# Kernel tuning notes

Measured on AMD Instinct MI355X. Metric: run time of the kernel, lower is better.

The kernel has to match this reference:

```python
import jax, jax.numpy as jnp
import numpy as np

NUM_HEADS = 8

def setup_inputs() -> dict:
    key = jax.random.key(0)
    ks = jax.random.split(key, 16)
    B, N, M, C = 4, 2048, 2048, 256
    Hd = 4 * C  # mlp hidden = dim * mlp_ratio
    std = 0.02
    x = jax.random.normal(ks[0], (B, N, C), dtype=jnp.float32)
    y = jax.random.normal(ks[1], (B, M, C), dtype=jnp.float32)
    token_types = jax.random.randint(ks[2], (B, N), 0, 2).astype(jnp.int64)
    token_types = token_types.at[0, 0].set(0)  # take the fresh-kv branch
    inp = {
        'x': x, 'y': y, 'token_types': token_types,
        'Wq': jax.random.normal(ks[3], (C, C)) * std,
        'Wkv': jax.random.normal(ks[4], (C, 2 * C)) * std,
        'Ws1': jax.random.normal(ks[5], (C, Hd)) * std,
        'bs1': jnp.zeros((Hd,)),
        'Ws2': jax.random.normal(ks[6], (Hd, C)) * std,
        'bs2': jnp.zeros((C,)),
        'Wl1': jax.random.normal(ks[7], (C, Hd)) * std,
        'bl1': jnp.zeros((Hd,)),
        'Wl2': jax.random.normal(ks[8], (Hd, C)) * std,
        'bl2': jnp.zeros((C,)),
    }
    return inp


def reference(x, y, token_types, Wq, Wkv, Ws1, bs1, Ws2, bs2, Wl1, bl1, Wl2, bl2):
    B, N, C = x.shape
    H = NUM_HEADS
    d = C // H
    scale = d ** -0.5
    # q: [B,H,N,d]
    q = (x @ Wq).reshape(B, N, H, d).transpose(0, 2, 1, 3)
    # kv: [B,M,2,H,d] -> k,v: [B,H,M,d]
    M = y.shape[1]
    kv = (y @ Wkv).reshape(B, M, 2, H, d)
    k = kv[:, :, 0].transpose(0, 2, 1, 3)
    v = kv[:, :, 1].transpose(0, 2, 1, 3)
    attn = jax.nn.softmax(jnp.einsum('bhnd,bhmd->bhnm', q, k) * scale, axis=-1)
    ctx = jnp.einsum('bhnm,bhmd->bhnd', attn, v)  # [B,H,N,d]
    ctx = ctx.transpose(0, 2, 1, 3).reshape(B, N, C)
    # MoE MLP: expert_s for token_type==0, expert_l for token_type==1
    out_s = jax.nn.gelu(ctx @ Ws1 + bs1, approximate=False) @ Ws2 + bs2
    out_l = jax.nn.gelu(ctx @ Wl1 + bl1, approximate=False) @ Wl2 + bl2
    is_l = (token_types == 1)[..., None]
    out = jnp.where(is_l, out_l, out_s)
    return out
```

## Files before the change

kernel.cpp:

```cpp
#include <hip/hip_runtime.h>

typedef unsigned short ushort_t;
typedef __attribute__((ext_vector_type(8))) short bf16x8;
typedef __attribute__((ext_vector_type(4))) short bf16x4;
typedef __attribute__((ext_vector_type(4))) float f32x4;

#define MFMA16(a, b, c) __builtin_amdgcn_mfma_f32_16x16x32_bf16(a, b, c, 0, 0, 0)

typedef const __attribute__((address_space(1))) void gvoid_t;
typedef __attribute__((address_space(3))) void lvoid_t;

__device__ __forceinline__ void glds16(const ushort_t* g, ushort_t* l) {
    __builtin_amdgcn_global_load_lds((gvoid_t*)(const void*)g, (lvoid_t*)(void*)l, 16, 0, 0);
}

__device__ inline ushort_t f2bf(float f) {
    union { float f; unsigned int i; } v;
    v.f = f;
    unsigned int r = v.i + 0x7FFFu + ((v.i >> 16) & 1u);
    return (ushort_t)(r >> 16);
}

__device__ __forceinline__ unsigned int cvtpk_bf16(float lo, float hi) {
    unsigned int r;
    asm("v_cvt_pk_bf16_f32 %0, %1, %2" : "=v"(r) : "v"(lo), "v"(hi));
    return r;
}

__device__ __forceinline__ float fexp2(float x) {
    float r;
    asm("v_exp_f32 %0, %1" : "=v"(r) : "v"(x));
    return r;
}

__device__ __forceinline__ float gelu_fast(float x) {
    float z = x * 0.70710678118654752f;
    float a = fabsf(z);
    float den = 1.0f + 0.3275911f * a;
    float tr;
    asm("v_rcp_f32 %0, %1" : "=v"(tr) : "v"(den));
    float poly = ((((1.061405429f * tr - 1.453152027f) * tr + 1.421413741f) * tr
                   - 0.284496736f) * tr + 0.254829592f) * tr;
    float e = fexp2(-z * z * 1.4426950408889634f);
    float erfa = 1.0f - poly * e;
    float erfv = copysignf(erfa, z);
    return 0.5f * x * (1.0f + erfv);
}

__global__ __launch_bounds__(256) void prep_k(
    const float* Wq, const float* Wkv, const float* Ws1,
    const float* Ws2, const float* Wl1, const float* Wl2,
    const float* x, const float* y, const int* tt,
    ushort_t* WqT, ushort_t* WkvT, ushort_t* Ws1T,
    ushort_t* Ws2T, ushort_t* Wl1T, ushort_t* Wl2T,
    ushort_t* xb, ushort_t* yb,
    int* perm0, int* perm1, int* cnt)
{
    const int job = blockIdx.y;
    const int t = threadIdx.x;
    if (job < 6) {
        __shared__ ushort_t lds[64][65];
        const float* src; ushort_t* dst; int R, Cc;
        switch (job) {
            case 0:  src = Wq;  dst = WqT;  R = 256;  Cc = 256;  break;
            case 1:  src = Wkv; dst = WkvT; R = 256;  Cc = 512;  break;
            case 2:  src = Ws1; dst = Ws1T; R = 256;  Cc = 1024; break;
            case 3:  src = Ws2; dst = Ws2T; R = 1024; Cc = 256;  break;
            case 4:  src = Wl1; dst = Wl1T; R = 256;  Cc = 1024; break;
            default: src = Wl2; dst = Wl2T; R = 1024; Cc = 256;  break;
        }
        const int ctiles = Cc >> 6;
        const int ntiles = (R >> 6) * ctiles;
        for (int tile = blockIdx.x; tile < ntiles; tile += gridDim.x) {
            const int r0 = (tile / ctiles) << 6, c0 = (tile - (tile / ctiles) * ctiles) << 6;
            #pragma unroll
            for (int it = 0; it < 16; ++it) {
                int idx = it * 256 + t;
                int rr = idx >> 6, cc = idx & 63;
                lds[rr][cc] = f2bf(src[(size_t)(r0 + rr) * Cc + c0 + cc]);
            }
            __syncthreads();
            #pragma unroll
            for (int it = 0; it < 16; ++it) {
                int idx = it * 256 + t;
                int rr = idx >> 6, cc = idx & 63;
                dst[(size_t)(c0 + rr) * R + r0 + cc] = lds[cc][rr];
            }
            __syncthreads();
        }
    } else if (job < 8) {
        const float* src = (job == 6) ? x : y;
        ushort_t* dst = (job == 6) ? xb : yb;
        const int tid = blockIdx.x * 256 + t;
        const int nth = gridDim.x * 256;
        for (int i = tid; i < (1 << 18); i += nth) {
            f32x4 a0 = *(const f32x4*)(src + (size_t)i * 8);
            f32x4 a1 = *(const f32x4*)(src + (size_t)i * 8 + 4);
            union { unsigned int u[4]; bf16x8 v; } o;
            o.u[0] = cvtpk_bf16(a0[0], a0[1]);
            o.u[1] = cvtpk_bf16(a0[2], a0[3]);
            o.u[2] = cvtpk_bf16(a1[0], a1[1]);
            o.u[3] = cvtpk_bf16(a1[2], a1[3]);
            *(bf16x8*)(dst + (size_t)i * 8) = o.v;
        }
    } else {
        if (blockIdx.x != 0) return;
        __shared__ int s0[256], s1[256];
        unsigned int mask = 0;
        #pragma unroll
        for (int j = 0; j < 8; ++j) {
            int4 v = *(const int4*)(tt + t * 32 + j * 4);
            mask |= (unsigned int)(v.x & 1) << (j * 4)
                  | (unsigned int)(v.y & 1) << (j * 4 + 1)
                  | (unsigned int)(v.z & 1) << (j * 4 + 2)
                  | (unsigned int)(v.w & 1) << (j * 4 + 3);
        }
        const int c1 = __popc(mask), c0 = 32 - c1;
        s0[t] = c0; s1[t] = c1;
        __syncthreads();
        for (int d = 1; d < 256; d <<= 1) {
            int a0 = 0, a1 = 0;
            if (t >= d) { a0 = s0[t - d]; a1 = s1[t - d]; }
            __syncthreads();
            s0[t] += a0; s1[t] += a1;
            __syncthreads();
        }
        const int tot0 = s0[255], tot1 = s1[255];
        int off0 = s0[t] - c0, off1 = s1[t] - c1;
        #pragma unroll
        for (int j = 0; j < 32; ++j) {
            int row = t * 32 + j;
            if ((mask >> j) & 1) perm1[off1++] = row;
            else                 perm0[off0++] = row;
        }
        for (int i = tot0 + t; i < 8320; i += 256) perm0[i] = 0;
        for (int i = tot1 + t; i < 8320; i += 256) perm1[i] = 0;
        if (t == 0) { cnt[0] = tot0; cnt[1] = tot1; }
    }
}

template<int ACT, int GATHER, int SCATTER, int OUTF32, int VSCATTER>
__device__ __forceinline__ void gemm_body(
    ushort_t* Als, ushort_t* Bls, int vbid,
    const ushort_t* __restrict__ A, const ushort_t* __restrict__ Bt,
    const float* __restrict__ bias, void* __restrict__ Cv,
    const int* __restrict__ perm, const int* __restrict__ ncnt,
    ushort_t* __restrict__ kpk, ushort_t* __restrict__ vpk,
    float oscale, int M, int N, int K, int aRowOff, int outRowOff)
{
    const int t = threadIdx.x;
    const int lane = t & 63, w = t >> 6;
    const int wr = w >> 1, wc = w & 1;
    const int ntn = N >> 7;
    const int mt = vbid / ntn, nt = vbid - mt * ntn;
    const int mbase = mt << 7, nbase = nt << 7;
    const int n16 = lane & 15, g = lane >> 4;

    int ne = M;
    if (GATHER || SCATTER) {
        ne = *ncnt;
        if (mbase >= ne) return;
    }

    int arow[4], skb[4], brow[4];
    #pragma unroll
    for (int j = 0; j < 4; ++j) {
        int p = j * 256 + t;
        int sr = p >> 3;
        skb[j] = (p & 7) ^ (sr & 7);
        brow[j] = sr;
        arow[j] = GATHER ? perm[mbase + sr] : (mbase + sr + aRowOff);
    }

    f32x4 acc[4][4];
    #pragma unroll
    for (int mi = 0; mi < 4; ++mi)
        #pragma unroll
        for (int ni = 0; ni < 4; ++ni) acc[mi][ni] = (f32x4){0.f, 0.f, 0.f, 0.f};

    for (int k0 = 0; k0 < K; k0 += 64) {
        #pragma unroll
        for (int j = 0; j < 4; ++j) {
            glds16(A + (size_t)arow[j] * K + k0 + skb[j] * 8, &Als[(j * 256 + t) * 8]);
            glds16(Bt + (size_t)(nbase + brow[j]) * K + k0 + skb[j] * 8, &Bls[(j * 256 + t) * 8]);
        }
        __syncthreads();
        #pragma unroll
        for (int ks = 0; ks < 2; ++ks) {
            bf16x8 af[4], bfr[4];
            #pragma unroll
            for (int i = 0; i < 4; ++i) {
                const int ar = wr * 64 + i * 16 + n16;
                af[i]  = *(const bf16x8*)&Als[ar * 64 + (((ks << 2) + g) ^ (ar & 7)) * 8];
                const int br = wc * 64 + i * 16 + n16;
                bfr[i] = *(const bf16x8*)&Bls[br * 64 + (((ks << 2) + g) ^ (br & 7)) * 8];
            }
            #pragma unroll
            for (int mi = 0; mi < 4; ++mi)
                #pragma unroll
                for (int ni = 0; ni < 4; ++ni)
                    acc[mi][ni] = MFMA16(af[mi], bfr[ni], acc[mi][ni]);
        }
        __syncthreads();
    }

    float bv[4];
    #pragma unroll
    for (int ni = 0; ni < 4; ++ni)
        bv[ni] = (bias != nullptr) ? bias[nbase + wc * 64 + ni * 16 + n16] : 0.f;

    #pragma unroll
    for (int mi = 0; mi < 4; ++mi) {
        #pragma unroll
        for (int r = 0; r < 4; ++r) {
            const int pos = mbase + wr * 64 + mi * 16 + (g << 2) + r;
            int orow = pos + outRowOff;
            if (GATHER || SCATTER) {
                if (pos >= ne) continue;
                if (SCATTER) orow = perm[pos];
            }
            #pragma unroll
            for (int ni = 0; ni < 4; ++ni) {
                const int col = nbase + wc * 64 + ni * 16 + n16;
                float v = (acc[mi][ni][r] + bv[ni]) * oscale;
                if (ACT) v = gelu_fast(v);
                if (VSCATTER) {
                    const int bb = pos >> 11, mm = pos & 2047;
                    if (col < 256) {
                        const int hh = col >> 5, dd = col & 31;
                        kpk[((size_t)(bb * 8 + hh) * 2048 + mm) * 32 + dd] = f2bf(v);
                    } else {
                        const int hh = (col - 256) >> 5, dd = (col - 256) & 31;
                        const int m31 = mm & 31;
                        const int kap = ((m31 >> 2) & 3) * 8 + ((m31 >> 4) & 1) * 4 + (m31 & 3);
                        vpk[(((size_t)(bb * 8 + hh) * 64 + (mm >> 5)) * 32 + dd) * 32 + kap] = f2bf(v);
                    }
                } else {
                    if (OUTF32) ((float*)Cv)[(size_t)orow * N + col] = v;
                    else ((ushort_t*)Cv)[(size_t)orow * N + col] = f2bf(v);
                }
            }
        }
    }
}

__global__ __launch_bounds__(256, 2) void qkv_k(
    const ushort_t* xb, const ushort_t* yb,
    const ushort_t* WqT, const ushort_t* WkvT,
    ushort_t* qws, ushort_t* kpk, ushort_t* vpk, float qscale)
{
    __shared__ ushort_t Als[128 * 64];
    __shared__ ushort_t Bls[128 * 64];
    if (blockIdx.x < 128) {
        gemm_body<0, 0, 0, 0, 0>(Als, Bls, blockIdx.x, xb, WqT, nullptr, qws,
                                 nullptr, nullptr, nullptr, nullptr,
                                 qscale, 8192, 256, 256, 0, 0);
    } else {
        gemm_body<0, 0, 0, 0, 1>(Als, Bls, blockIdx.x - 128, yb, WkvT, nullptr, nullptr,
                                 nullptr, nullptr, kpk, vpk,
                                 1.f, 8192, 512, 256, 0, 0);
    }
}

__global__ __launch_bounds__(256, 2) void mlp1_k(
    const ushort_t* ctx, const ushort_t* Ws1T, const ushort_t* Wl1T,
    const float* bs1, const float* bl1, ushort_t* hws,
    const int* perm0, const int* perm1, const int* cnt)
{
    __shared__ ushort_t Als[128 * 64];
    __shared__ ushort_t Bls[128 * 64];
    const int half = blockIdx.x >> 9, vbid = blockIdx.x & 511;
    const int outOff = half ? cnt[0] : 0;
    gemm_body<1, 1, 0, 0, 0>(Als, Bls, vbid, ctx, half ? Wl1T : Ws1T,
                             half ? bl1 : bs1, hws,
                             half ? perm1 : perm0, cnt + half, nullptr, nullptr,
                             1.f, 8192, 1024, 256, 0, outOff);
}

__global__ __launch_bounds__(256, 2) void mlp2_k(
    const ushort_t* hws, const ushort_t* Ws2T, const ushort_t* Wl2T,
    const float* bs2, const float* bl2, float* out,
    const int* perm0, const int* perm1, const int* cnt)
{
    __shared__ ushort_t Als[128 * 64];
    __shared__ ushort_t Bls[128 * 64];
    const int half = blockIdx.x >> 7, vbid = blockIdx.x & 127;
    const int aOff = half ? cnt[0] : 0;
    gemm_body<0, 0, 1, 1, 0>(Als, Bls, vbid, hws, half ? Wl2T : Ws2T,
                             half ? bl2 : bs2, out,
                             half ? perm1 : perm0, cnt + half, nullptr, nullptr,
                             1.f, 8192, 256, 1024, aOff, 0);
}

__global__ __launch_bounds__(256, 2) void attn_k(
    const ushort_t* __restrict__ q, const ushort_t* __restrict__ kpack,
    const ushort_t* __restrict__ vpack, ushort_t* __restrict__ ctx)
{
    __shared__ ushort_t KV[4096];

    const int t = threadIdx.x, lane = t & 63, w = t >> 6;
    const int bid = (blockIdx.x & 7) * 64 + (blockIdx.x >> 3);
    const int tile = bid & 15, bh = bid >> 4, b = bh >> 3, h = bh & 7;
    const int n16 = lane & 15, g = lane >> 4, lk = g << 3;
    const int row0 = tile * 128 + w * 32;

    const ushort_t* qp = q + ((size_t)(b * 2048 + row0 + n16) * 256 + h * 32 + lk);
    const bf16x8 qf0 = *(const bf16x8*)qp;
    const bf16x8 qf1 = *(const bf16x8*)(qp + 16 * 256);

    const ushort_t* kg = kpack + (size_t)bh * 65536 + t * 8;
    const ushort_t* vg = vpack + (size_t)bh * 65536 + t * 8;

    f32x4 a0d0 = {0.f, 0.f, 0.f, 0.f}, a0d1 = {0.f, 0.f, 0.f, 0.f};
    f32x4 a1d0 = {0.f, 0.f, 0.f, 0.f}, a1d1 = {0.f, 0.f, 0.f, 0.f};
    f32x4 den0 = {0.f, 0.f, 0.f, 0.f}, den1 = {0.f, 0.f, 0.f, 0.f};
    const f32x4 zero = {0.f, 0.f, 0.f, 0.f};
    bf16x8 ones;
    #pragma unroll
    for (int e = 0; e < 8; ++e) ones[e] = (short)0x3F80;

    const int kOff = n16 * 32 + lk;
    const int vOff = 2048 + n16 * 32 + lk;

    bf16x8 kreg = *(const bf16x8*)kg;
    bf16x8 vreg = *(const bf16x8*)vg;
    *(bf16x8*)&KV[t * 8] = kreg;
    *(bf16x8*)&KV[2048 + t * 8] = vreg;

    for (int it = 0; it < 32; ++it) {
        __syncthreads();
        if (it + 1 < 32) {
            kreg = *(const bf16x8*)(kg + (size_t)(it + 1) * 2048);
            vreg = *(const bf16x8*)(vg + (size_t)(it + 1) * 2048);
        }

        bf16x8 kf[4], vf[4];
        #pragma unroll
        for (int i = 0; i < 4; ++i) {
            kf[i] = *(const bf16x8*)&KV[kOff + i * 512];
            vf[i] = *(const bf16x8*)&KV[vOff + i * 512];
        }

        f32x4 st0[4], st1[4];
        __builtin_amdgcn_s_setprio(1);
        #pragma unroll
        for (int mt = 0; mt < 4; ++mt) {
            st0[mt] = MFMA16(kf[mt], qf0, zero);
            st1[mt] = MFMA16(kf[mt], qf1, zero);
        }
        __builtin_amdgcn_s_setprio(0);

        float p0[4][4], p1[4][4];
        #pragma unroll
        for (int mt = 0; mt < 4; ++mt) {
            #pragma unroll
            for (int r = 0; r < 4; ++r) {
                p0[mt][r] = fexp2(st0[mt][r]);
                p1[mt][r] = fexp2(st1[mt][r]);
            }
        }

        __builtin_amdgcn_s_setprio(1);
        #pragma unroll
        for (int kpn = 0; kpn < 2; ++kpn) {
            union { unsigned int u[4]; bf16x8 v; } pb0, pb1;
            pb0.u[0] = cvtpk_bf16(p0[2 * kpn][0], p0[2 * kpn][1]);
            pb0.u[1] = cvtpk_bf16(p0[2 * kpn][2], p0[2 * kpn][3]);
            pb0.u[2] = cvtpk_bf16(p0[2 * kpn + 1][0], p0[2 * kpn + 1][1]);
            pb0.u[3] = cvtpk_bf16(p0[2 * kpn + 1][2], p0[2 * kpn + 1][3]);
            pb1.u[0] = cvtpk_bf16(p1[2 * kpn][0], p1[2 * kpn][1]);
            pb1.u[1] = cvtpk_bf16(p1[2 * kpn][2], p1[2 * kpn][3]);
            pb1.u[2] = cvtpk_bf16(p1[2 * kpn + 1][0], p1[2 * kpn + 1][1]);
            pb1.u[3] = cvtpk_bf16(p1[2 * kpn + 1][2], p1[2 * kpn + 1][3]);
            a0d0 = MFMA16(vf[2 * kpn],     pb0.v, a0d0);
            a0d1 = MFMA16(vf[2 * kpn + 1], pb0.v, a0d1);
            a1d0 = MFMA16(vf[2 * kpn],     pb1.v, a1d0);
            a1d1 = MFMA16(vf[2 * kpn + 1], pb1.v, a1d1);
            den0 = MFMA16(ones, pb0.v, den0);
            den1 = MFMA16(ones, pb1.v, den1);
        }
        __builtin_amdgcn_s_setprio(0);

        __syncthreads();
        if (it + 1 < 32) {
            *(bf16x8*)&KV[t * 8] = kreg;
            *(bf16x8*)&KV[2048 + t * 8] = vreg;
        }
    }

    const float i0 = 1.f / den0[0], i1 = 1.f / den1[0];
    bf16x4 s00, s01, s10, s11;
    #pragma unroll
    for (int r = 0; r < 4; ++r) {
        s00[r] = (short)f2bf(a0d0[r] * i0);
        s01[r] = (short)f2bf(a0d1[r] * i0);
        s10[r] = (short)f2bf(a1d0[r] * i1);
        s11[r] = (short)f2bf(a1d1[r] * i1);
    }
    ushort_t* op0 = ctx + (size_t)(b * 2048 + row0 + n16) * 256 + h * 32;
    ushort_t* op1 = op0 + 16 * 256;
    *(bf16x4*)(op0 + 4 * g)      = s00;
    *(bf16x4*)(op0 + 16 + 4 * g) = s01;
    *(bf16x4*)(op1 + 4 * g)      = s10;
    *(bf16x4*)(op1 + 16 + 4 * g) = s11;
}

extern "C" void kernel_launch(void* const* d_in, const int* in_sizes, int n_in,
                              void* d_out, int out_size, void* d_ws, size_t ws_size,
                              hipStream_t stream)
{
    const float* x   = (const float*)d_in[0];
    const float* y   = (const float*)d_in[1];
    const int*   tt  = (const int*)d_in[2];
    const float* Wq  = (const float*)d_in[3];
    const float* Wkv = (const float*)d_in[4];
    const float* Ws1 = (const float*)d_in[5];
    const float* bs1 = (const float*)d_in[6];
    const float* Ws2 = (const float*)d_in[7];
    const float* bs2 = (const float*)d_in[8];
    const float* Wl1 = (const float*)d_in[9];
    const float* bl1 = (const float*)d_in[10];
    const float* Wl2 = (const float*)d_in[11];
    const float* bl2 = (const float*)d_in[12];
    float* out = (float*)d_out;
    ushort_t* ws = (ushort_t*)d_ws;

    ushort_t* WqT   = ws;
    ushort_t* WkvT  = WqT  + 65536;
    ushort_t* Ws1T  = WkvT + 131072;
    ushort_t* Ws2T  = Ws1T + 262144;
    ushort_t* Wl1T  = Ws2T + 262144;
    ushort_t* Wl2T  = Wl1T + 262144;
    ushort_t* kpws  = Wl2T + 262144;
    ushort_t* vtws  = kpws + (size_t)8192 * 512;
    ushort_t* ctxws = vtws + 2097152;
    ushort_t* regA  = ctxws + 2097152;
    ushort_t* xbf   = regA;
    ushort_t* ybf   = xbf + 2097152;
    ushort_t* qws   = ybf + 2097152;
    ushort_t* hws   = regA;
    int* iws   = (int*)(ws + (size_t)18022400);
    int* perm0 = iws;
    int* perm1 = iws + 8320;
    int* cnt   = iws + 16640;

    const float qscale = 0.17677669529663687f * 1.4426950408889634f;

    prep_k<<<dim3(64, 9), 256, 0, stream>>>(Wq, Wkv, Ws1, Ws2, Wl1, Wl2, x, y, tt,
                                            WqT, WkvT, Ws1T, Ws2T, Wl1T, Wl2T,
                                            xbf, ybf, perm0, perm1, cnt);

    qkv_k<<<dim3(384), 256, 0, stream>>>(xbf, ybf, WqT, WkvT, qws, kpws, vtws, qscale);

    attn_k<<<dim3(512), 256, 0, stream>>>(qws, kpws, vtws, ctxws);

    mlp1_k<<<dim3(1024), 256, 0, stream>>>(ctxws, Ws1T, Wl1T, bs1, bl1, hws,
                                           perm0, perm1, cnt);
    mlp2_k<<<dim3(256), 256, 0, stream>>>(hws, Ws2T, Wl2T, bs2, bl2, out,
                                          perm0, perm1, cnt);
}
```

Before: 91.90 us.

## Fuse fp32-to-bf16 input conversion into QKV GEMM and double-buffer attention KV

```diff
diff --git a/kernel.cpp b/kernel.cpp
--- a/kernel.cpp
+++ b/kernel.cpp
@@ -50,10 +50,9 @@
 __global__ __launch_bounds__(256) void prep_k(
     const float* Wq, const float* Wkv, const float* Ws1,
     const float* Ws2, const float* Wl1, const float* Wl2,
-    const float* x, const float* y, const int* tt,
+    const int* tt,
     ushort_t* WqT, ushort_t* WkvT, ushort_t* Ws1T,
     ushort_t* Ws2T, ushort_t* Wl1T, ushort_t* Wl2T,
-    ushort_t* xb, ushort_t* yb,
     int* perm0, int* perm1, int* cnt)
 {
     const int job = blockIdx.y;
@@ -88,21 +87,6 @@
             }
             __syncthreads();
         }
-    } else if (job < 8) {
-        const float* src = (job == 6) ? x : y;
-        ushort_t* dst = (job == 6) ? xb : yb;
-        const int tid = blockIdx.x * 256 + t;
-        const int nth = gridDim.x * 256;
-        for (int i = tid; i < (1 << 18); i += nth) {
-            f32x4 a0 = *(const f32x4*)(src + (size_t)i * 8);
-            f32x4 a1 = *(const f32x4*)(src + (size_t)i * 8 + 4);
-            union { unsigned int u[4]; bf16x8 v; } o;
-            o.u[0] = cvtpk_bf16(a0[0], a0[1]);
-            o.u[1] = cvtpk_bf16(a0[2], a0[3]);
-            o.u[2] = cvtpk_bf16(a1[0], a1[1]);
-            o.u[3] = cvtpk_bf16(a1[2], a1[3]);
-            *(bf16x8*)(dst + (size_t)i * 8) = o.v;
-        }
     } else {
         if (blockIdx.x != 0) return;
         __shared__ int s0[256], s1[256];
@@ -139,10 +123,10 @@
     }
 }
 
-template<int ACT, int GATHER, int SCATTER, int OUTF32, int VSCATTER>
+template<int ACT, int GATHER, int SCATTER, int OUTF32, int VSCATTER, int AF32>
 __device__ __forceinline__ void gemm_body(
     ushort_t* Als, ushort_t* Bls, int vbid,
-    const ushort_t* __restrict__ A, const ushort_t* __restrict__ Bt,
+    const void* __restrict__ Av, const ushort_t* __restrict__ Bt,
     const float* __restrict__ bias, void* __restrict__ Cv,
     const int* __restrict__ perm, const int* __restrict__ ncnt,
     ushort_t* __restrict__ kpk, ushort_t* __restrict__ vpk,
@@ -181,8 +165,22 @@
     for (int k0 = 0; k0 < K; k0 += 64) {
         #pragma unroll
         for (int j = 0; j < 4; ++j) {
-            glds16(A + (size_t)arow[j] * K + k0 + skb[j] * 8, &Als[(j * 256 + t) * 8]);
-            glds16(Bt + (size_t)(nbase + brow[j]) * K + k0 + skb[j] * 8, &Bls[(j * 256 + t) * 8]);
+            if (AF32) {
+                const float* ap = (const float*)Av + (size_t)arow[j] * K + k0 + skb[j] * 8;
+                f32x4 a0 = *(const f32x4*)ap;
+                f32x4 a1 = *(const f32x4*)(ap + 4);
+                union { unsigned int u[4]; bf16x8 v; } pk;
+                pk.u[0] = cvtpk_bf16(a0[0], a0[1]);
+                pk.u[1] = cvtpk_bf16(a0[2], a0[3]);
+                pk.u[2] = cvtpk_bf16(a1[0], a1[1]);
+                pk.u[3] = cvtpk_bf16(a1[2], a1[3]);
+                *(bf16x8*)&Als[(j * 256 + t) * 8] = pk.v;
+            } else {
+                glds16((const ushort_t*)Av + (size_t)arow[j] * K + k0 + skb[j] * 8,
+                       &Als[(j * 256 + t) * 8]);
+            }
+            glds16(Bt + (size_t)(nbase + brow[j]) * K + k0 + skb[j] * 8,
+                   &Bls[(j * 256 + t) * 8]);
         }
         __syncthreads();
         #pragma unroll
@@ -245,20 +243,20 @@
 }
 
 __global__ __launch_bounds__(256, 2) void qkv_k(
-    const ushort_t* xb, const ushort_t* yb,
+    const float* x, const float* y,
     const ushort_t* WqT, const ushort_t* WkvT,
     ushort_t* qws, ushort_t* kpk, ushort_t* vpk, float qscale)
 {
     __shared__ ushort_t Als[128 * 64];
     __shared__ ushort_t Bls[128 * 64];
     if (blockIdx.x < 128) {
-        gemm_body<0, 0, 0, 0, 0>(Als, Bls, blockIdx.x, xb, WqT, nullptr, qws,
-                                 nullptr, nullptr, nullptr, nullptr,
-                                 qscale, 8192, 256, 256, 0, 0);
+        gemm_body<0, 0, 0, 0, 0, 1>(Als, Bls, blockIdx.x, x, WqT, nullptr, qws,
+                                    nullptr, nullptr, nullptr, nullptr,
+                                    qscale, 8192, 256, 256, 0, 0);
     } else {
-        gemm_body<0, 0, 0, 0, 1>(Als, Bls, blockIdx.x - 128, yb, WkvT, nullptr, nullptr,
-                                 nullptr, nullptr, kpk, vpk,
-                                 1.f, 8192, 512, 256, 0, 0);
+        gemm_body<0, 0, 0, 0, 1, 1>(Als, Bls, blockIdx.x - 128, y, WkvT, nullptr, nullptr,
+                                    nullptr, nullptr, kpk, vpk,
+                                    1.f, 8192, 512, 256, 0, 0);
     }
 }
 
@@ -271,10 +269,10 @@
     __shared__ ushort_t Bls[128 * 64];
     const int half = blockIdx.x >> 9, vbid = blockIdx.x & 511;
     const int outOff = half ? cnt[0] : 0;
-    gemm_body<1, 1, 0, 0, 0>(Als, Bls, vbid, ctx, half ? Wl1T : Ws1T,
-                             half ? bl1 : bs1, hws,
-                             half ? perm1 : perm0, cnt + half, nullptr, nullptr,
-                             1.f, 8192, 1024, 256, 0, outOff);
+    gemm_body<1, 1, 0, 0, 0, 0>(Als, Bls, vbid, ctx, half ? Wl1T : Ws1T,
+                                half ? bl1 : bs1, hws,
+                                half ? perm1 : perm0, cnt + half, nullptr, nullptr,
+                                1.f, 8192, 1024, 256, 0, outOff);
 }
 
 __global__ __launch_bounds__(256, 2) void mlp2_k(
@@ -286,17 +284,17 @@
     __shared__ ushort_t Bls[128 * 64];
     const int half = blockIdx.x >> 7, vbid = blockIdx.x & 127;
     const int aOff = half ? cnt[0] : 0;
-    gemm_body<0, 0, 1, 1, 0>(Als, Bls, vbid, hws, half ? Wl2T : Ws2T,
-                             half ? bl2 : bs2, out,
-                             half ? perm1 : perm0, cnt + half, nullptr, nullptr,
-                             1.f, 8192, 256, 1024, aOff, 0);
+    gemm_body<0, 0, 1, 1, 0, 0>(Als, Bls, vbid, hws, half ? Wl2T : Ws2T,
+                                half ? bl2 : bs2, out,
+                                half ? perm1 : perm0, cnt + half, nullptr, nullptr,
+                                1.f, 8192, 256, 1024, aOff, 0);
 }
 
 __global__ __launch_bounds__(256, 2) void attn_k(
     const ushort_t* __restrict__ q, const ushort_t* __restrict__ kpack,
     const ushort_t* __restrict__ vpack, ushort_t* __restrict__ ctx)
 {
-    __shared__ ushort_t KV[4096];
+    __shared__ ushort_t KV[2][4096];
 
     const int t = threadIdx.x, lane = t & 63, w = t >> 6;
     const int bid = (blockIdx.x & 7) * 64 + (blockIdx.x >> 3);
@@ -324,9 +322,10 @@
 
     bf16x8 kreg = *(const bf16x8*)kg;
     bf16x8 vreg = *(const bf16x8*)vg;
-    *(bf16x8*)&KV[t * 8] = kreg;
-    *(bf16x8*)&KV[2048 + t * 8] = vreg;
-
+    *(bf16x8*)&KV[0][t * 8] = kreg;
+    *(bf16x8*)&KV[0][2048 + t * 8] = vreg;
+
+    int cur = 0;
     for (int it = 0; it < 32; ++it) {
         __syncthreads();
         if (it + 1 < 32) {
@@ -337,8 +336,8 @@
         bf16x8 kf[4], vf[4];
         #pragma unroll
         for (int i = 0; i < 4; ++i) {
-            kf[i] = *(const bf16x8*)&KV[kOff + i * 512];
-            vf[i] = *(const bf16x8*)&KV[vOff + i * 512];
+            kf[i] = *(const bf16x8*)&KV[cur][kOff + i * 512];
+            vf[i] = *(const bf16x8*)&KV[cur][vOff + i * 512];
         }
 
         f32x4 st0[4], st1[4];
@@ -381,11 +380,11 @@
         }
         __builtin_amdgcn_s_setprio(0);
 
-        __syncthreads();
         if (it + 1 < 32) {
-            *(bf16x8*)&KV[t * 8] = kreg;
-            *(bf16x8*)&KV[2048 + t * 8] = vreg;
-        }
+            *(bf16x8*)&KV[cur ^ 1][t * 8] = kreg;
+            *(bf16x8*)&KV[cur ^ 1][2048 + t * 8] = vreg;
+        }
+        cur ^= 1;
     }
 
     const float i0 = 1.f / den0[0], i1 = 1.f / den1[0];
@@ -435,9 +434,7 @@
     ushort_t* vtws  = kpws + (size_t)8192 * 512;
     ushort_t* ctxws = vtws + 2097152;
     ushort_t* regA  = ctxws + 2097152;
-    ushort_t* xbf   = regA;
-    ushort_t* ybf   = xbf + 2097152;
-    ushort_t* qws   = ybf + 2097152;
+    ushort_t* qws   = regA + 4194304;
     ushort_t* hws   = regA;
     int* iws   = (int*)(ws + (size_t)18022400);
     int* perm0 = iws;
@@ -446,11 +443,11 @@
 
     const float qscale = 0.17677669529663687f * 1.4426950408889634f;
 
-    prep_k<<<dim3(64, 9), 256, 0, stream>>>(Wq, Wkv, Ws1, Ws2, Wl1, Wl2, x, y, tt,
+    prep_k<<<dim3(64, 7), 256, 0, stream>>>(Wq, Wkv, Ws1, Ws2, Wl1, Wl2, tt,
                                             WqT, WkvT, Ws1T, Ws2T, Wl1T, Wl2T,
-                                            xbf, ybf, perm0, perm1, cnt);
-
-    qkv_k<<<dim3(384), 256, 0, stream>>>(xbf, ybf, WqT, WkvT, qws, kpws, vtws, qscale);
+                                            perm0, perm1, cnt);
+
+    qkv_k<<<dim3(384), 256, 0, stream>>>(x, y, WqT, WkvT, qws, kpws, vtws, qscale);
 
     attn_k<<<dim3(512), 256, 0, stream>>>(qws, kpws, vtws, ctxws);
 
```

Result: slower. 97.20 us (+5.8%).
